# Performance work log

Measured on AMD Instinct MI355X. Metric: run time of the kernel, lower is better.

Reference implementation:

```python
import jax, jax.numpy as jnp
from jax import lax
import numpy as np

K = 32        # self.k: neighbors queried per center
TOP = 5       # inner topk size (hardcoded in source)
MAX_ITER = 16 # bound on the data-dependent while loop; leftovers emitted at final iter


def _refine_one(pc, centers, ids):
    """Vectorized translation of the per-batch while-loop.

    Instead of shrinking the sample set each iteration (data-dependent shape),
    every sample is tracked with an `active` flag and a convergence-iteration
    stamp. Emitting order in the torch code is (iteration, surviving-order),
    and boolean masking preserves relative original order, so a stable sort by
    (conv_iter, original_index) reproduces the exact concatenation order.
    """
    N, D = pc.shape
    S = centers.shape[0]
    ar = jnp.arange(S)

    def knn(q):  # q: [S,3] -> [S,K] indices of nearest cloud points (ascending dist)
        d2 = jnp.sum((q[:, None, :] - pc[None, :, :]) ** 2, axis=-1)  # [S,N]
        _, ind = lax.top_k(-d2, K)
        return ind

    def step(cur_pts, cur_idx):
        ind = knn(cur_pts)                                   # [S,K]
        nbh = pc[ind]                                        # [S,K,3]
        gc = jnp.mean(nbh, axis=1)                           # [S,3]
        dist = jnp.linalg.norm(nbh - gc[:, None, :], axis=2) # [S,K]
        _, top = lax.top_k(-dist, TOP)                       # [S,TOP] smallest dists
        in_top = jnp.any(top == 0, axis=1)                   # center (col 0) stable?
        new_idx = ind[ar, top[:, 0]]                         # point closest to centroid
        return ind, in_top, new_idx

    def body(it, st):
        cur_pts, cur_idx, conv_it, out_pts, out_idx, out_grp, active = st
        ind, in_top, new_idx = step(cur_pts, cur_idx)
        newly = active & in_top
        conv_it = jnp.where(newly, it, conv_it)
        out_pts = jnp.where(newly[:, None], cur_pts, out_pts)
        out_idx = jnp.where(newly, cur_idx, out_idx)
        out_grp = jnp.where(newly[:, None], ind, out_grp)
        move = active & ~in_top
        cur_idx = jnp.where(move, new_idx, cur_idx)
        cur_pts = jnp.where(move[:, None], pc[new_idx], cur_pts)
        return (cur_pts, cur_idx, conv_it, out_pts, out_idx, out_grp, move)

    st0 = (centers, ids,
           jnp.full((S,), MAX_ITER, jnp.int32),
           jnp.zeros((S, D), pc.dtype),
           jnp.zeros((S,), ids.dtype),
           jnp.zeros((S, K), jnp.int32),
           jnp.ones((S,), bool))
    cur_pts, cur_idx, conv_it, out_pts, out_idx, out_grp, active = lax.fori_loop(
        0, MAX_ITER, body, st0)

    # force-emit any sample that never converged within MAX_ITER
    ind, _, _ = step(cur_pts, cur_idx)
    out_pts = jnp.where(active[:, None], cur_pts, out_pts)
    out_idx = jnp.where(active, cur_idx, out_idx)
    out_grp = jnp.where(active[:, None], ind, out_grp)

    order = jnp.argsort(conv_it * (S + 1) + ar)  # stable (iter, orig-pos) order
    return out_pts[order], out_idx[order], out_grp[order]


def setup_inputs() -> dict:
    key = jax.random.key(0)
    k1, k2, k3 = jax.random.split(key, 3)
    B, N, S = 8, 8192, 1024
    xyz = jax.random.normal(k1, (B, N, 3), jnp.float32)
    center = jax.random.normal(k2, (B, S, 3), jnp.float32)
    idx = jax.random.randint(k3, (B, S), 0, N, jnp.int32)
    return {"xyz": xyz, "center": center, "idx": idx}


def reference(xyz, center, idx):
    assert xyz.shape[0] == center.shape[0]
    C, I1, I2 = jax.vmap(_refine_one)(xyz, center, idx)
    # torch runs under no_grad; outputs are detached constants
    return (lax.stop_gradient(C), I1, I2)
```

## Files before the change

### kernel.cpp

```cpp
#include <hip/hip_runtime.h>
#include <stdint.h>

#define BATCH   8
#define NPTS    8192
#define SCH     1024
#define KNN     32
#define TOPC    5
#define MAXIT   16
#define NCELL   4096
#define NGRP    128
#define NSEED   6

typedef unsigned long long ull;
typedef uint16_t u16;
typedef float vf2 __attribute__((ext_vector_type(2)));
typedef float vf4 __attribute__((ext_vector_type(4)));

#define SENTKEY ((((ull)0x7F800000u) << 13) | 0x1FFFull)

__device__ __forceinline__ float d2_exact(vf4 q, vf4 p) {
#pragma clang fp contract(off)
    vf2 d = q.xy - p.xy;
    vf2 s = d * d;
    float dz = q.z - p.z;
    float sz = dz * dz;
    return (s.x + s.y) + sz;
}

__device__ __forceinline__ void insert_top4(ull key, ull& k0, ull& k1, ull& k2,
                                            ull& k3, float& th) {
    if (key < k3) {
        k3 = key;
        { bool c = k3 < k2; ull mn = c ? k3 : k2, mx = c ? k2 : k3; k2 = mn; k3 = mx; }
        { bool c = k2 < k1; ull mn = c ? k2 : k1, mx = c ? k1 : k2; k1 = mn; k2 = mx; }
        { bool c = k1 < k0; ull mn = c ? k1 : k0, mx = c ? k0 : k1; k0 = mn; k1 = mx; }
        th = __uint_as_float((uint32_t)(k3 >> 13));
    }
}

__device__ __forceinline__ ull wave_min_u64(ull k) {
#pragma unroll
    for (int off = 32; off; off >>= 1) {
        ull o = (ull)__shfl_xor((unsigned long long)k, off, 64);
        k = o < k ? o : k;
    }
    return k;
}
__device__ __forceinline__ ull wave_max_u64(ull k) {
#pragma unroll
    for (int off = 32; off; off >>= 1) {
        ull o = (ull)__shfl_xor((unsigned long long)k, off, 64);
        k = o > k ? o : k;
    }
    return k;
}

__device__ __forceinline__ float bbox_mind2(vf4 q, vf4 c, vf4 h) {
    float dx = fmaxf(fabsf(q.x - c.x) - h.x, 0.f);
    float dy = fmaxf(fabsf(q.y - c.y) - h.y, 0.f);
    float dz = fmaxf(fabsf(q.z - c.z) - h.z, 0.f);
    return (dx * dx + dy * dy + dz * dz) * 0.9999f;
}

__device__ __forceinline__ ull cx(ull v, int xl, bool keepmin) {
    ull o = (ull)__shfl_xor((unsigned long long)v, xl, 64);
    return ((v < o) == keepmin) ? v : o;
}
__device__ __forceinline__ void cswap(ull& a, ull& b, bool up) {
    bool lt = a < b;
    ull mn = lt ? a : b, mx = lt ? b : a;
    a = up ? mn : mx;
    b = up ? mx : mn;
}

__device__ __forceinline__ void sort128(ull& s0, ull& s1, int lane) {
    cswap(s0, s1, true);
    if (lane & 1) { ull t = s0; s0 = s1; s1 = t; }
#pragma unroll
    for (int kk = 4; kk <= 128; kk <<= 1) {
        const bool up = (lane & (kk >> 1)) == 0;
#pragma unroll
        for (int d = kk >> 1; d >= 2; d >>= 1) {
            const int xl = d >> 1;
            const bool keepmin = (up == ((lane & xl) == 0));
            s0 = cx(s0, xl, keepmin);
            s1 = cx(s1, xl, keepmin);
        }
        cswap(s0, s1, up);
    }
}

__device__ __forceinline__ int next_gid(ull& r0, ull& r1) {
    if (r0) { int g = __ffsll((unsigned long long)r0) - 1; r0 &= r0 - 1; return g; }
    if (r1) { int g = __ffsll((unsigned long long)r1) - 1; r1 &= r1 - 1; return 64 + g; }
    return -1;
}

__device__ __forceinline__ int cell_of(float x, float y, float z) {
    int cxi = min(15, max(0, (int)floorf((x + 4.0f) * 2.0f)));
    int cyi = min(15, max(0, (int)floorf((y + 4.0f) * 2.0f)));
    int czi = min(15, max(0, (int)floorf((z + 4.0f) * 2.0f)));
    uint32_t sx = (cxi & 1) | ((cxi & 2) << 2) | ((cxi & 4) << 4) | ((cxi & 8) << 6);
    uint32_t sy = (cyi & 1) | ((cyi & 2) << 2) | ((cyi & 4) << 4) | ((cyi & 8) << 6);
    uint32_t sz = (czi & 1) | ((czi & 2) << 2) | ((czi & 4) << 4) | ((czi & 8) << 6);
    return (int)(sx | (sy << 1) | (sz << 2));
}

__device__ __attribute__((noinline)) int serial_topk_masked(
    const vf4* __restrict__ Psort, vf4 q, int lane, ull sm0, ull sm1) {
    ull k0 = SENTKEY, k1 = SENTKEY, k2 = SENTKEY, k3 = SENTKEY;
    int s0 = 0, s1 = 0, s2 = 0, s3 = 0;
    float th = __builtin_inff();
    for (int gid = 0; gid < NGRP; ++gid) {
        bool sel = (gid < 64) ? ((sm0 >> gid) & 1ull) : ((sm1 >> (gid - 64)) & 1ull);
        if (!sel) continue;
        vf4 p = Psort[(gid << 6) + lane];
        float d2 = d2_exact(q, p);
        uint32_t oi = __float_as_uint(p.w);
        ull key = ((ull)__float_as_uint(d2) << 13) | oi;
        if (d2 <= th && key < k3) {
            k3 = key; s3 = gid;
            if (k3 < k2) { ull t = k2; k2 = k3; k3 = t; int ts = s2; s2 = s3; s3 = ts; }
            if (k2 < k1) { ull t = k1; k1 = k2; k2 = t; int ts = s1; s1 = s2; s2 = ts; }
            if (k1 < k0) { ull t = k0; k0 = k1; k1 = t; int ts = s0; s0 = s1; s1 = ts; }
            th = __uint_as_float((uint32_t)(k3 >> 13));
        }
    }
    ull em0 = 0ull, em1 = 0ull;
    int cnt = 4, my_ind = 0;
    for (int r = 0; r < KNN; ++r) {
        ull gmin = wave_min_u64(k0);
        int widx = (int)(gmin & 0x1FFFull);
        if (lane == r) my_ind = widx;
        if (k0 == gmin) {
            int g = s0;
            if (g < 64) em0 |= 1ull << g; else em1 |= 1ull << (g - 64);
            k0 = k1; k1 = k2; k2 = k3; k3 = SENTKEY;
            s0 = s1; s1 = s2; s2 = s3;
            if (--cnt == 0) {
                k0 = k1 = k2 = k3 = SENTKEY;
                float th2 = __builtin_inff();
                for (int gid = 0; gid < NGRP; ++gid) {
                    bool sel = (gid < 64) ? ((sm0 >> gid) & 1ull)
                                          : ((sm1 >> (gid - 64)) & 1ull);
                    bool ex = (gid < 64) ? ((em0 >> gid) & 1ull)
                                         : ((em1 >> (gid - 64)) & 1ull);
                    if (!sel || ex) continue;
                    vf4 p = Psort[(gid << 6) + lane];
                    float d2 = d2_exact(q, p);
                    uint32_t oi = __float_as_uint(p.w);
                    ull key = ((ull)__float_as_uint(d2) << 13) | oi;
                    if (d2 <= th2 && key < k3) {
                        k3 = key; s3 = gid;
                        if (k3 < k2) { ull t = k2; k2 = k3; k3 = t; int ts = s2; s2 = s3; s3 = ts; }
                        if (k2 < k1) { ull t = k1; k1 = k2; k2 = t; int ts = s1; s1 = s2; s2 = ts; }
                        if (k1 < k0) { ull t = k0; k0 = k1; k1 = t; int ts = s0; s0 = s1; s1 = ts; }
                        th2 = __uint_as_float((uint32_t)(k3 >> 13));
                    }
                }
                cnt = 4;
            }
        }
    }
    return my_ind;
}

__global__ __launch_bounds__(256) void prep_kernel(const float* __restrict__ xyz,
                                                   vf4* __restrict__ pc4,
                                                   int* __restrict__ counts) {
    int i = (int)(blockIdx.x * blockDim.x + threadIdx.x);
    if (i >= BATCH * NPTS) return;
    vf4 v;
    v.x = xyz[(size_t)i * 3 + 0];
    v.y = xyz[(size_t)i * 3 + 1];
    v.z = xyz[(size_t)i * 3 + 2];
    v.w = 0.f;
    pc4[i] = v;
    int b = i >> 13;
    atomicAdd(&counts[b * NCELL + cell_of(v.x, v.y, v.z)], 1);
}

__global__ __launch_bounds__(1024) void scan_kernel(const int* __restrict__ counts,
                                                    int* __restrict__ cursor) {
    int b = (int)blockIdx.x, tid = (int)threadIdx.x;
    __shared__ int part[1024];
    int base = b * NCELL + tid * 4;
    int v0 = counts[base], v1 = counts[base + 1], v2 = counts[base + 2], v3 = counts[base + 3];
    int s = v0 + v1 + v2 + v3;
    part[tid] = s;
    __syncthreads();
    for (int off = 1; off < 1024; off <<= 1) {
        int t = (tid >= off) ? part[tid - off] : 0;
        __syncthreads();
        part[tid] += t;
        __syncthreads();
    }
    int excl = part[tid] - s;
    cursor[base] = excl;
    cursor[base + 1] = excl + v0;
    cursor[base + 2] = excl + v0 + v1;
    cursor[base + 3] = excl + v0 + v1 + v2;
}

__global__ __launch_bounds__(256) void scatter_kernel(const vf4* __restrict__ pc4,
                                                      int* __restrict__ cursor,
                                                      vf4* __restrict__ sortedP) {
    int i = (int)(blockIdx.x * blockDim.x + threadIdx.x);
    if (i >= BATCH * NPTS) return;
    vf4 v = pc4[i];
    int b = i >> 13, pi = i & (NPTS - 1);
    int c = cell_of(v.x, v.y, v.z);
    int pos = atomicAdd(&cursor[b * NCELL + c], 1);
    v.w = __uint_as_float((uint32_t)pi);
    sortedP[((size_t)b << 13) + pos] = v;
}

__global__ __launch_bounds__(256) void bbox_kernel(const vf4* __restrict__ sortedP,
                                                   vf4* __restrict__ bC,
                                                   vf4* __restrict__ bH) {
    int g = (int)((blockIdx.x * blockDim.x + threadIdx.x) >> 6);
    int lane = (int)(threadIdx.x & 63);
    vf4 p = sortedP[((size_t)g << 6) + lane];
    float mnx = p.x, mxx = p.x, mny = p.y, mxy = p.y, mnz = p.z, mxz = p.z;
#pragma unroll
    for (int off = 32; off; off >>= 1) {
        mnx = fminf(mnx, __shfl_xor(mnx, off, 64));
        mxx = fmaxf(mxx, __shfl_xor(mxx, off, 64));
        mny = fminf(mny, __shfl_xor(mny, off, 64));
        mxy = fmaxf(mxy, __shfl_xor(mxy, off, 64));
        mnz = fminf(mnz, __shfl_xor(mnz, off, 64));
        mxz = fmaxf(mxz, __shfl_xor(mxz, off, 64));
    }
    if (lane == 0) {
        vf4 c, h;
        c.x = (mnx + mxx) * 0.5f; c.y = (mny + mxy) * 0.5f; c.z = (mnz + mxz) * 0.5f; c.w = 0.f;
        h.x = (mxx - mnx) * 0.5f; h.y = (mxy - mny) * 0.5f; h.z = (mxz - mnz) * 0.5f; h.w = 0.f;
        bC[g] = c;
        bH[g] = h;
    }
}

__global__ __launch_bounds__(256) void refine_kernel(
    const vf4* __restrict__ pc4, const vf4* __restrict__ sortedP,
    const vf4* __restrict__ bC, const vf4* __restrict__ bH,
    const float* __restrict__ center, const int* __restrict__ idx_in,
    float* __restrict__ pts_ws, int* __restrict__ idx_ws,
    int* __restrict__ grp_ws, int* __restrict__ conv_ws) {
    const int lane = (int)(threadIdx.x & 63);
    const int w = (int)(threadIdx.x >> 6);
    const int wv = (int)((blockIdx.x * blockDim.x + threadIdx.x) >> 6);
    const int b = (int)(blockIdx.x >> 8);
    const vf4* __restrict__ Porig = pc4 + ((size_t)b << 13);
    const vf4* __restrict__ Psort = sortedP + ((size_t)b << 13);

    __shared__ vf4 sbC[NGRP], sbH[NGRP];
    __shared__ vf4 nbh[4][KNN];

    {
        const int t = (int)threadIdx.x;
        if (t < NGRP) sbC[t] = bC[(b << 7) + t];
        else          sbH[t - NGRP] = bH[(b << 7) + (t - NGRP)];
    }
    __syncthreads();

    const size_t ch = (size_t)wv;
    vf4 q;
    q.x = center[ch * 3 + 0];
    q.y = center[ch * 3 + 1];
    q.z = center[ch * 3 + 2];
    q.w = 0.f;
    int qidx = idx_in[ch];

    int conv = MAXIT;
    int my_ind = 0;
    vf4 myp = q;
    bool warm = false;

    for (int it = 0;; ++it) {
        const vf4 c0 = sbC[lane],      h0 = sbH[lane];
        const vf4 c1 = sbC[64 + lane], h1 = sbH[64 + lane];
        const float m0 = bbox_mind2(q, c0, h0);
        const float m1 = bbox_mind2(q, c1, h1);

        ull k0 = SENTKEY, k1 = SENTKEY, k2 = SENTKEY, k3 = SENTKEY;
        float th = __builtin_inff();
        ull sm0 = 0ull, sm1 = 0ull, am0 = 0ull, am1 = 0ull;
        float th0 = __builtin_inff();

        bool fastwarm = false;
        if (warm) {
            const float dw = (lane < KNN) ? d2_exact(q, myp) : 0.f;
            th0 = dw;
#pragma unroll
            for (int off = 32; off; off >>= 1)
                th0 = fmaxf(th0, __shfl_xor(th0, off, 64));
            sm0 = __ballot(m0 <= th0);
            sm1 = __ballot(m1 <= th0);
            const int nsel = __popcll(sm0) + __popcll(sm1);
            if (nsel <= 20) { fastwarm = true; am0 = sm0; am1 = sm1; }
        }

        if (!fastwarm) {
            sm0 = 0ull; sm1 = 0ull;
            ull g0k = ((ull)__float_as_uint(m0) << 7) | (uint32_t)lane;
            ull g1k = ((ull)__float_as_uint(m1) << 7) | (uint32_t)(64 + lane);
            sort128(g0k, g1k, lane);
#pragma unroll
            for (int r = 0; r < NSEED; ++r) {
                const ull nk = (r & 1)
                    ? (ull)__shfl((unsigned long long)g1k, r >> 1, 64)
                    : (ull)__shfl((unsigned long long)g0k, r >> 1, 64);
                const int gid = (int)(nk & 127ull);
                if (gid < 64) sm0 |= 1ull << gid; else sm1 |= 1ull << (gid - 64);
                const vf4 p = Psort[(gid << 6) + lane];
                const float d2 = d2_exact(q, p);
                if (d2 <= th)
                    insert_top4(((ull)__float_as_uint(d2) << 13) | __float_as_uint(p.w),
                                k0, k1, k2, k3, th);
            }
            ull t = k0;
            {
                ull o = (ull)__shfl_xor((unsigned long long)t, 32, 64);
                t = o < t ? o : t;
            }
            const ull B = wave_max_u64(t);
            const float Bd = fminf(__uint_as_float((uint32_t)(B >> 13)), th0);
            am0 = __ballot(m0 <= Bd) & ~sm0;
            am1 = __ballot(m1 <= Bd) & ~sm1;
            sm0 |= am0; sm1 |= am1;
        }

        {
            ull rem0 = am0, rem1 = am1;
            int ga = next_gid(rem0, rem1);
            while (ga >= 0) {
                const int gb = next_gid(rem0, rem1);
                const vf4 pa = Psort[(ga << 6) + lane];
                vf4 pb;
                if (gb >= 0) pb = Psort[(gb << 6) + lane];
                const float da = d2_exact(q, pa);
                if (da <= th)
                    insert_top4(((ull)__float_as_uint(da) << 13) | __float_as_uint(pa.w),
                                k0, k1, k2, k3, th);
                if (gb >= 0) {
                    const float dbv = d2_exact(q, pb);
                    if (dbv <= th)
                        insert_top4(((ull)__float_as_uint(dbv) << 13) | __float_as_uint(pb.w),
                                    k0, k1, k2, k3, th);
                }
                ga = next_gid(rem0, rem1);
            }
        }
        const ull prek3 = k3;

        const bool odd = (lane & 1) != 0;
        ull a0 = odd ? k3 : k0;
        ull a1 = odd ? k2 : k1;
        ull a2 = odd ? k1 : k2;
        ull a3 = odd ? k0 : k3;
#pragma unroll
        for (int kk = 8; kk <= 256; kk <<= 1) {
            const bool up = (lane & (kk >> 2)) == 0;
#pragma unroll
            for (int d = kk >> 1; d >= 4; d >>= 1) {
                const int xl = d >> 2;
                const bool keepmin = (up == ((lane & xl) == 0));
                a0 = cx(a0, xl, keepmin);
                a1 = cx(a1, xl, keepmin);
                a2 = cx(a2, xl, keepmin);
                a3 = cx(a3, xl, keepmin);
            }
            cswap(a0, a2, up); cswap(a1, a3, up);
            cswap(a0, a1, up); cswap(a2, a3, up);
        }
        const ull tau = (ull)__shfl((unsigned long long)a3, 7, 64);
        const ull bad = __ballot(prek3 < tau);
        if (bad != 0ull) {
            my_ind = serial_topk_masked(Psort, q, lane, sm0, sm1);
        } else {
            const int src = lane >> 2;
            const uint32_t lo0 = (uint32_t)__shfl((int)(uint32_t)a0, src, 64);
            const uint32_t lo1 = (uint32_t)__shfl((int)(uint32_t)a1, src, 64);
            const uint32_t lo2 = (uint32_t)__shfl((int)(uint32_t)a2, src, 64);
            const uint32_t lo3 = (uint32_t)__shfl((int)(uint32_t)a3, src, 64);
            const int sel = lane & 3;
            uint32_t lo = (sel == 0) ? lo0 : (sel == 1) ? lo1 : (sel == 2) ? lo2 : lo3;
            my_ind = (int)(lo & 0x1FFFu);
        }

        if (it == MAXIT) break;

        myp = q;
        if (lane < KNN) {
            myp = Porig[my_ind];
            nbh[w][lane] = myp;
        }
        __asm__ volatile("s_waitcnt lgkmcnt(0)" ::: "memory");
        float sx = 0.f, sy = 0.f, sz = 0.f;
#pragma unroll
        for (int j = 0; j < KNN; ++j) {
            vf4 pj = nbh[w][j];
            sx = __fadd_rn(sx, pj.x);
            sy = __fadd_rn(sy, pj.y);
            sz = __fadd_rn(sz, pj.z);
        }
        const float gx = __fmul_rn(sx, 0.03125f);
        const float gy = __fmul_rn(sy, 0.03125f);
        const float gz = __fmul_rn(sz, 0.03125f);

        float dj = __builtin_inff();
        if (lane < KNN) {
            const float dx = __fsub_rn(myp.x, gx);
            const float dy = __fsub_rn(myp.y, gy);
            const float dz = __fsub_rn(myp.z, gz);
            dj = sqrtf(__fadd_rn(__fadd_rn(__fmul_rn(dx, dx), __fmul_rn(dy, dy)),
                                 __fmul_rn(dz, dz)));
        }
        const uint32_t db = __float_as_uint(dj);
        const uint32_t d0 = (uint32_t)__shfl((int)db, 0, 64);
        const ull bal = __ballot(db < d0);
        if (__popcll(bal) <= TOPC - 1) { conv = it; break; }

        uint32_t m = db;
#pragma unroll
        for (int off = 32; off; off >>= 1) {
            uint32_t o = (uint32_t)__shfl_xor((int)m, off, 64);
            m = o < m ? o : m;
        }
        const ull balm = __ballot(db == m);
        const int jm = __ffsll((unsigned long long)balm) - 1;
        qidx = __shfl(my_ind, jm, 64);
        q.x = __shfl(myp.x, jm, 64);
        q.y = __shfl(myp.y, jm, 64);
        q.z = __shfl(myp.z, jm, 64);
        q.w = 0.f;
        warm = true;
    }

    if (lane < KNN) grp_ws[ch * KNN + lane] = my_ind;
    if (lane == 0) {
        pts_ws[ch * 3 + 0] = q.x;
        pts_ws[ch * 3 + 1] = q.y;
        pts_ws[ch * 3 + 2] = q.z;
        idx_ws[ch] = qidx;
        conv_ws[ch] = conv;
    }
}

__global__ __launch_bounds__(1024) void order_kernel(
    const float* __restrict__ pts_ws, const int* __restrict__ idx_ws,
    const int* __restrict__ grp_ws, const int* __restrict__ conv_ws,
    float* __restrict__ out) {
    const int b = (int)blockIdx.x;
    const int s = (int)threadIdx.x;
    const int w = s >> 6, l = s & 63;
    __shared__ int wavecnt[16][MAXIT + 1];
    __shared__ int binbase[MAXIT + 1];
    const size_t ch = (size_t)b * SCH + s;
    const int c = conv_ws[ch];
    int rw = 0;
#pragma unroll
    for (int v = 0; v <= MAXIT; ++v) {
        ull bal = __ballot(c == v);
        if (l == 0) wavecnt[w][v] = (int)__popcll(bal);
        if (c == v) rw = (int)__popcll(bal & ((1ull << l) - 1ull));
    }
    __syncthreads();
    if (s == 0) {
        int acc = 0;
        for (int v = 0; v <= MAXIT; ++v) {
            int t = 0;
            for (int w2 = 0; w2 < 16; ++w2) t += wavecnt[w2][v];
            binbase[v] = acc;
            acc += t;
        }
    }
    __syncthreads();
    int pos = binbase[c] + rw;
    for (int w2 = 0; w2 < w; ++w2) pos += wavecnt[w2][c];

    float* __restrict__ C  = out;
    float* __restrict__ I1 = out + (size_t)BATCH * SCH * 3;
    float* __restrict__ I2 = I1 + (size_t)BATCH * SCH;
    const size_t o = (size_t)b * SCH + pos;
    C[o * 3 + 0] = pts_ws[ch * 3 + 0];
    C[o * 3 + 1] = pts_ws[ch * 3 + 1];
    C[o * 3 + 2] = pts_ws[ch * 3 + 2];
    I1[o] = (float)idx_ws[ch];
#pragma unroll
    for (int k = 0; k < KNN; ++k) I2[o * KNN + k] = (float)grp_ws[ch * KNN + k];
}

extern "C" void kernel_launch(void* const* d_in, const int* in_sizes, int n_in,
                              void* d_out, int out_size, void* d_ws, size_t ws_size,
                              hipStream_t stream) {
    const float* xyz    = (const float*)d_in[0];
    const float* center = (const float*)d_in[1];
    const int*   idx_in = (const int*)d_in[2];
    float* out = (float*)d_out;

    char* wp = (char*)d_ws;
    vf4* pc4     = (vf4*)wp;  wp += (size_t)BATCH * NPTS * sizeof(vf4);
    vf4* sortedP = (vf4*)wp;  wp += (size_t)BATCH * NPTS * sizeof(vf4);
    vf4* bC      = (vf4*)wp;  wp += (size_t)BATCH * NGRP * sizeof(vf4);
    vf4* bH      = (vf4*)wp;  wp += (size_t)BATCH * NGRP * sizeof(vf4);
    int* counts  = (int*)wp;  wp += (size_t)BATCH * NCELL * 4;
    int* cursor  = (int*)wp;  wp += (size_t)BATCH * NCELL * 4;
    float* pts_ws = (float*)wp; wp += (size_t)BATCH * SCH * 3 * 4;
    int*   idx_ws = (int*)wp;   wp += (size_t)BATCH * SCH * 4;
    int*   grp_ws = (int*)wp;   wp += (size_t)BATCH * SCH * KNN * 4;
    int*   conv_ws = (int*)wp;

    hipMemsetAsync(counts, 0, (size_t)BATCH * NCELL * 4, stream);
    prep_kernel<<<(BATCH * NPTS + 255) / 256, 256, 0, stream>>>(xyz, pc4, counts);
    scan_kernel<<<BATCH, 1024, 0, stream>>>(counts, cursor);
    scatter_kernel<<<(BATCH * NPTS + 255) / 256, 256, 0, stream>>>(pc4, cursor, sortedP);
    bbox_kernel<<<(BATCH * NGRP * 64) / 256, 256, 0, stream>>>(sortedP, bC, bH);

    const int chains = BATCH * SCH;
    refine_kernel<<<chains * 64 / 256, 256, 0, stream>>>(
        pc4, sortedP, bC, bH, center, idx_in, pts_ws, idx_ws, grp_ws, conv_ws);
    order_kernel<<<BATCH, SCH, 0, stream>>>(pts_ws, idx_ws, grp_ws, conv_ws, out);
}
```

Before: 203.1 us.

## Use DPP shuffles, 32-bit group sort keys, interleaved batch mapping, waves-per-EU hint

Swaps the xor-1 and xor-2 cross-lane shuffles for DPP quad permutes instead of LDS-backed bpermute. It also shrinks the 128-entry bitonic sort of bounding-box keys from 64-bit to 32-bit keys by dropping the low mantissa bits. Blocks are remapped so consecutive blocks cycle through batches, and a waves-per-EU attribute is added to steer register allocation. Truncated keys may reorder nearly tied groups during seed selection, which should only affect pruning efficiency, not correctness.

Measured after the change: 191.4 us. 5.8% less time.

```diff
diff --git a/kernel.cpp b/kernel.cpp
--- a/kernel.cpp
+++ b/kernel.cpp
@@ -12,11 +12,26 @@
 #define NSEED   6
 
 typedef unsigned long long ull;
-typedef uint16_t u16;
 typedef float vf2 __attribute__((ext_vector_type(2)));
 typedef float vf4 __attribute__((ext_vector_type(4)));
 
 #define SENTKEY ((((ull)0x7F800000u) << 13) | 0x1FFFull)
+
+__device__ __forceinline__ uint32_t xshfl32(uint32_t v, int xl) {
+    if (xl == 1)
+        return (uint32_t)__builtin_amdgcn_update_dpp((int)v, (int)v, 0xB1, 0xF, 0xF, true);
+    if (xl == 2)
+        return (uint32_t)__builtin_amdgcn_update_dpp((int)v, (int)v, 0x4E, 0xF, 0xF, true);
+    return (uint32_t)__shfl_xor((int)v, xl, 64);
+}
+__device__ __forceinline__ ull xshfl64(ull v, int xl) {
+    uint32_t lo = xshfl32((uint32_t)v, xl);
+    uint32_t hi = xshfl32((uint32_t)(v >> 32), xl);
+    return ((ull)hi << 32) | lo;
+}
+__device__ __forceinline__ float xshflf(float v, int xl) {
+    return __uint_as_float(xshfl32(__float_as_uint(v), xl));
+}
 
 __device__ __forceinline__ float d2_exact(vf4 q, vf4 p) {
 #pragma clang fp contract(off)
@@ -41,7 +56,7 @@
 __device__ __forceinline__ ull wave_min_u64(ull k) {
 #pragma unroll
     for (int off = 32; off; off >>= 1) {
-        ull o = (ull)__shfl_xor((unsigned long long)k, off, 64);
+        ull o = xshfl64(k, off);
         k = o < k ? o : k;
     }
     return k;
@@ -49,7 +64,7 @@
 __device__ __forceinline__ ull wave_max_u64(ull k) {
 #pragma unroll
     for (int off = 32; off; off >>= 1) {
-        ull o = (ull)__shfl_xor((unsigned long long)k, off, 64);
+        ull o = xshfl64(k, off);
         k = o > k ? o : k;
     }
     return k;
@@ -63,7 +78,7 @@
 }
 
 __device__ __forceinline__ ull cx(ull v, int xl, bool keepmin) {
-    ull o = (ull)__shfl_xor((unsigned long long)v, xl, 64);
+    ull o = xshfl64(v, xl);
     return ((v < o) == keepmin) ? v : o;
 }
 __device__ __forceinline__ void cswap(ull& a, ull& b, bool up) {
@@ -73,9 +88,19 @@
     b = up ? mx : mn;
 }
 
-__device__ __forceinline__ void sort128(ull& s0, ull& s1, int lane) {
-    cswap(s0, s1, true);
-    if (lane & 1) { ull t = s0; s0 = s1; s1 = t; }
+__device__ __forceinline__ uint32_t cx32(uint32_t v, int xl, bool keepmin) {
+    uint32_t o = xshfl32(v, xl);
+    return ((v < o) == keepmin) ? v : o;
+}
+__device__ __forceinline__ void cswap32(uint32_t& a, uint32_t& b, bool up) {
+    uint32_t mn = a < b ? a : b, mx = a < b ? b : a;
+    a = up ? mn : mx;
+    b = up ? mx : mn;
+}
+
+__device__ __forceinline__ void sort128_u32(uint32_t& s0, uint32_t& s1, int lane) {
+    cswap32(s0, s1, true);
+    if (lane & 1) { uint32_t t = s0; s0 = s1; s1 = t; }
 #pragma unroll
     for (int kk = 4; kk <= 128; kk <<= 1) {
         const bool up = (lane & (kk >> 1)) == 0;
@@ -83,10 +108,10 @@
         for (int d = kk >> 1; d >= 2; d >>= 1) {
             const int xl = d >> 1;
             const bool keepmin = (up == ((lane & xl) == 0));
-            s0 = cx(s0, xl, keepmin);
-            s1 = cx(s1, xl, keepmin);
-        }
-        cswap(s0, s1, up);
+            s0 = cx32(s0, xl, keepmin);
+            s1 = cx32(s1, xl, keepmin);
+        }
+        cswap32(s0, s1, up);
     }
 }
 
@@ -224,12 +249,12 @@
     float mnx = p.x, mxx = p.x, mny = p.y, mxy = p.y, mnz = p.z, mxz = p.z;
 #pragma unroll
     for (int off = 32; off; off >>= 1) {
-        mnx = fminf(mnx, __shfl_xor(mnx, off, 64));
-        mxx = fmaxf(mxx, __shfl_xor(mxx, off, 64));
-        mny = fminf(mny, __shfl_xor(mny, off, 64));
-        mxy = fmaxf(mxy, __shfl_xor(mxy, off, 64));
-        mnz = fminf(mnz, __shfl_xor(mnz, off, 64));
-        mxz = fmaxf(mxz, __shfl_xor(mxz, off, 64));
+        mnx = fminf(mnx, xshflf(mnx, off));
+        mxx = fmaxf(mxx, xshflf(mxx, off));
+        mny = fminf(mny, xshflf(mny, off));
+        mxy = fmaxf(mxy, xshflf(mxy, off));
+        mnz = fminf(mnz, xshflf(mnz, off));
+        mxz = fmaxf(mxz, xshflf(mxz, off));
     }
     if (lane == 0) {
         vf4 c, h;
@@ -240,7 +265,9 @@
     }
 }
 
-__global__ __launch_bounds__(256) void refine_kernel(
+__global__ __launch_bounds__(256)
+__attribute__((amdgpu_waves_per_eu(2, 4)))
+void refine_kernel(
     const vf4* __restrict__ pc4, const vf4* __restrict__ sortedP,
     const vf4* __restrict__ bC, const vf4* __restrict__ bH,
     const float* __restrict__ center, const int* __restrict__ idx_in,
@@ -248,8 +275,8 @@
     int* __restrict__ grp_ws, int* __restrict__ conv_ws) {
     const int lane = (int)(threadIdx.x & 63);
     const int w = (int)(threadIdx.x >> 6);
-    const int wv = (int)((blockIdx.x * blockDim.x + threadIdx.x) >> 6);
-    const int b = (int)(blockIdx.x >> 8);
+    const int b = (int)(blockIdx.x & 7);
+    const int s = (((int)blockIdx.x >> 3) << 2) + w;
     const vf4* __restrict__ Porig = pc4 + ((size_t)b << 13);
     const vf4* __restrict__ Psort = sortedP + ((size_t)b << 13);
 
@@ -263,7 +290,7 @@
     }
     __syncthreads();
 
-    const size_t ch = (size_t)wv;
+    const size_t ch = ((size_t)b << 10) + (size_t)s;
     vf4 q;
     q.x = center[ch * 3 + 0];
     q.y = center[ch * 3 + 1];
@@ -293,7 +320,7 @@
             th0 = dw;
 #pragma unroll
             for (int off = 32; off; off >>= 1)
-                th0 = fmaxf(th0, __shfl_xor(th0, off, 64));
+                th0 = fmaxf(th0, xshflf(th0, off));
             sm0 = __ballot(m0 <= th0);
             sm1 = __ballot(m1 <= th0);
             const int nsel = __popcll(sm0) + __popcll(sm1);
@@ -302,15 +329,15 @@
 
         if (!fastwarm) {
             sm0 = 0ull; sm1 = 0ull;
-            ull g0k = ((ull)__float_as_uint(m0) << 7) | (uint32_t)lane;
-            ull g1k = ((ull)__float_as_uint(m1) << 7) | (uint32_t)(64 + lane);
-            sort128(g0k, g1k, lane);
+            uint32_t g0k = ((__float_as_uint(m0) >> 6) << 7) | (uint32_t)lane;
+            uint32_t g1k = ((__float_as_uint(m1) >> 6) << 7) | (uint32_t)(64 + lane);
+            sort128_u32(g0k, g1k, lane);
 #pragma unroll
             for (int r = 0; r < NSEED; ++r) {
-                const ull nk = (r & 1)
-                    ? (ull)__shfl((unsigned long long)g1k, r >> 1, 64)
-                    : (ull)__shfl((unsigned long long)g0k, r >> 1, 64);
-                const int gid = (int)(nk & 127ull);
+                const uint32_t nk = (r & 1)
+                    ? (uint32_t)__shfl((int)g1k, r >> 1, 64)
+                    : (uint32_t)__shfl((int)g0k, r >> 1, 64);
+                const int gid = (int)(nk & 127u);
                 if (gid < 64) sm0 |= 1ull << gid; else sm1 |= 1ull << (gid - 64);
                 const vf4 p = Psort[(gid << 6) + lane];
                 const float d2 = d2_exact(q, p);
@@ -320,7 +347,7 @@
             }
             ull t = k0;
             {
-                ull o = (ull)__shfl_xor((unsigned long long)t, 32, 64);
+                ull o = xshfl64(t, 32);
                 t = o < t ? o : t;
             }
             const ull B = wave_max_u64(t);
@@ -424,7 +451,7 @@
         uint32_t m = db;
 #pragma unroll
         for (int off = 32; off; off >>= 1) {
-            uint32_t o = (uint32_t)__shfl_xor((int)m, off, 64);
+            uint32_t o = xshfl32(m, off);
             m = o < m ? o : m;
         }
         const ull balm = __ballot(db == m);
```
